# Kernel tuning notes

Hardware: AMD Instinct MI355X
Metric: run time of the kernel (lower is better)

## Reference

```python
import jax, jax.numpy as jnp
import numpy as np

B, S, H, K = 64, 512, 768, 21  # batch, seq_len, bert hidden, num_labels


def setup_inputs() -> dict:
    key = jax.random.key(0)
    ks = jax.random.split(key, 8)
    hidden = jax.random.normal(ks[0], (B, S, H), jnp.float32)  # post-BERT states
    W = jax.random.normal(ks[1], (H, K), jnp.float32) * 0.02    # classifier weight
    b = jnp.zeros((K,), jnp.float32)                            # classifier bias
    start_transitions = jax.random.uniform(ks[2], (K,), jnp.float32, -0.1, 0.1)
    transitions = jax.random.uniform(ks[3], (K, K), jnp.float32, -0.1, 0.1)
    end_transitions = jax.random.uniform(ks[4], (K,), jnp.float32, -0.1, 0.1)
    labels = jax.random.randint(ks[5], (B, S), 0, K)
    # torchcrf requires mask[:, 0] == 1; use variable-length prefix masks
    lengths = jax.random.randint(ks[6], (B,), S // 2, S + 1)
    attention_mask = jnp.arange(S)[None, :] < lengths[:, None]  # [B,S] bool
    return dict(hidden=hidden, W=W, b=b,
                start_transitions=start_transitions,
                transitions=transitions,
                end_transitions=end_transitions,
                labels=labels, attention_mask=attention_mask)


def _crf_nll(logits, labels, mask, start_t, trans, end_t):
    """torchcrf CRF forward (reduction='sum' log-likelihood), negated."""
    fmask = mask.astype(logits.dtype)  # [B,S]
    # ---- numerator: score of the gold path ----
    emit = jnp.take_along_axis(logits, labels[..., None], axis=2)[..., 0]  # [B,S]
    tr = trans[labels[:, :-1], labels[:, 1:]]                              # [B,S-1]
    num = start_t[labels[:, 0]] + emit[:, 0] \
        + jnp.sum((emit[:, 1:] + tr) * fmask[:, 1:], axis=1)
    lengths = mask.sum(axis=1)
    last_tags = jnp.take_along_axis(labels, (lengths - 1)[:, None], axis=1)[:, 0]
    num = num + end_t[last_tags]
    # ---- denominator: forward algorithm (logsumexp recurrence) ----
    alpha0 = start_t[None, :] + logits[:, 0]           # [B,K]
    ems = jnp.swapaxes(logits[:, 1:], 0, 1)            # [S-1,B,K]
    ms = jnp.swapaxes(mask[:, 1:], 0, 1)               # [S-1,B]

    def step(alpha, xs):
        em, m = xs
        nxt = jax.scipy.special.logsumexp(
            alpha[:, :, None] + trans[None, :, :] + em[:, None, :], axis=1)
        return jnp.where(m[:, None], nxt, alpha), None

    alpha, _ = jax.lax.scan(step, alpha0, (ems, ms))
    logZ = jax.scipy.special.logsumexp(alpha + end_t[None, :], axis=1)  # [B]
    return jnp.sum(logZ - num)  # negative log-likelihood (sum over batch)


def reference(hidden, W, b, start_transitions, transitions, end_transitions,
              labels, attention_mask):
    # dropout is identity in eval; the GRU in __init__ is unused in forward
    logits = hidden @ W + b  # [B,S,K]
    nll = _crf_nll(logits, labels, attention_mask,
                   start_transitions, transitions, end_transitions)
    # module returns (logits, -1 * log_likelihood) = (logits, nll)
    return (logits, nll)
```

## Files before the change

kernel.cpp:

```cpp
#include <hip/hip_runtime.h>

#define BSZ 64
#define SEQ 512
#define HID 768
#define NK  21
#define NSEG 64
#define SEGLEN 8

typedef short bf16x8 __attribute__((ext_vector_type(8)));
typedef float f32x4  __attribute__((ext_vector_type(4)));

__device__ __forceinline__ unsigned f2bf1(float x) {
    unsigned u = __float_as_uint(x);
    return (u + 0x7fffu + ((u >> 16) & 1u)) >> 16;
}
__device__ __forceinline__ unsigned f2bf_pk(float lo, float hi) {
    return f2bf1(lo) | (f2bf1(hi) << 16);
}

__global__ __launch_bounds__(256) void wconv_kernel(
    const float* __restrict__ W, unsigned short* __restrict__ WT)
{
    const int idx = blockIdx.x * 256 + threadIdx.x;
    const int n = idx / HID;
    const int k = idx - n * HID;
    unsigned short v = 0;
    if (n < NK) v = (unsigned short)f2bf1(W[(size_t)k * NK + n]);
    WT[idx] = v;
}

__global__ __launch_bounds__(256) void gemm_bias_kernel(
    const float* __restrict__ hidden, const unsigned short* __restrict__ WT,
    const float* __restrict__ bias, float* __restrict__ out)
{
    const int tid  = threadIdx.x;
    const int lane = tid & 63;
    const int wv   = tid >> 6;
    const int n    = lane & 15;
    const int quad = lane >> 4;

    const int arow = blockIdx.x * 64 + wv * 16 + n;
    const float* ap = hidden + (size_t)arow * HID + quad * 8;
    const bf16x8* bp0 = (const bf16x8*)(WT + (size_t)n * HID + quad * 8);
    const bf16x8* bp1 = (const bf16x8*)(WT + (size_t)(16 + n) * HID + quad * 8);

    f32x4 acc0 = {0.f, 0.f, 0.f, 0.f};
    f32x4 acc1 = {0.f, 0.f, 0.f, 0.f};

    float4 c0a = *(const float4*)(ap + 0);
    float4 c0b = *(const float4*)(ap + 4);

    #pragma unroll
    for (int c = 0; c < HID / 32; ++c) {
        float4 c1a, c1b;
        if (c + 1 < HID / 32) {
            c1a = *(const float4*)(ap + (c + 1) * 32);
            c1b = *(const float4*)(ap + (c + 1) * 32 + 4);
        }
        union { bf16x8 v; unsigned u[4]; } af;
        af.u[0] = f2bf_pk(c0a.x, c0a.y);
        af.u[1] = f2bf_pk(c0a.z, c0a.w);
        af.u[2] = f2bf_pk(c0b.x, c0b.y);
        af.u[3] = f2bf_pk(c0b.z, c0b.w);

        const bf16x8 b0 = bp0[c * 4];
        const bf16x8 b1 = bp1[c * 4];

        acc0 = __builtin_amdgcn_mfma_f32_16x16x32_bf16(af.v, b0, acc0, 0, 0, 0);
        acc1 = __builtin_amdgcn_mfma_f32_16x16x32_bf16(af.v, b1, acc1, 0, 0, 0);
        c0a = c1a; c0b = c1b;
    }

    const float b0v = bias[n];
    const float b1v = (n < NK - 16) ? bias[16 + n] : 0.f;
    const int rbase = blockIdx.x * 64 + wv * 16 + quad * 4;
    #pragma unroll
    for (int r = 0; r < 4; ++r) {
        float* op = out + (size_t)(rbase + r) * NK;
        op[n] = acc0[r] + b0v;
        if (n < NK - 16) op[16 + n] = acc1[r] + b1v;
    }
}

__global__ __launch_bounds__(64) void prepass_kernel(
    const float* __restrict__ logits, const float* __restrict__ trans,
    const int* __restrict__ mask,
    float* __restrict__ Nrow, float* __restrict__ Ncol,
    float* __restrict__ rlog)
{
    const int bs   = blockIdx.x;
    const int b    = bs >> 6;
    const int s    = bs & 63;
    const int lane = threadIdx.x;
    int g = lane / 21; if (g > 2) g = 2;
    int i = lane - g * 21; if (i > 20) i = 20;
    const int j0 = 7 * g;

    const int* msk = mask + b * SEQ;
    int cnt = 0;
    #pragma unroll
    for (int t = 0; t < SEQ / 64; ++t) cnt += (msk[lane + 64 * t] != 0);
    #pragma unroll
    for (int off = 32; off > 0; off >>= 1) cnt += __shfl_xor(cnt, off, 64);
    const int L = cnt;

    float E[21][7];
    #pragma unroll
    for (int k = 0; k < 21; ++k)
        #pragma unroll
        for (int jl = 0; jl < 7; ++jl)
            E[k][jl] = __expf(trans[k * NK + j0 + jl]);

    const float* lg = logits + (size_t)b * SEQ * NK;

    float P[7];
    float rl = 0.f;
    const int t0 = s * SEGLEN + 1;

    if (t0 < L) {
        const float C = lg[t0 * NK];
        #pragma unroll
        for (int jl = 0; jl < 7; ++jl)
            P[jl] = E[i][jl] * __expf(lg[t0 * NK + j0 + jl] - C);
    } else {
        #pragma unroll
        for (int jl = 0; jl < 7; ++jl) P[jl] = (i == j0 + jl) ? 1.f : 0.f;
    }

#define BPF(v, idx) __uint_as_float(__builtin_amdgcn_ds_bpermute((idx) * 4, __float_as_uint(v)))

    #pragma unroll
    for (int u = 1; u < SEGLEN; ++u) {
        const int t = t0 + u;
        if (t < L) {
            float row[21];
            #pragma unroll
            for (int k = 0; k < 21; ++k)
                row[k] = BPF(P[k % 7], (k / 7) * 21 + i);

            const float C = lg[t * NK];
            float X[7];
            #pragma unroll
            for (int jl = 0; jl < 7; ++jl)
                X[jl] = __expf(lg[t * NK + j0 + jl] - C);

            #pragma unroll
            for (int jl = 0; jl < 7; ++jl) {
                float s0 = row[0] * E[0][jl];
                float s1 = row[1] * E[1][jl];
                float s2 = row[2] * E[2][jl];
                #pragma unroll
                for (int k = 3; k < 21; k += 3) {
                    s0 = fmaf(row[k    ], E[k    ][jl], s0);
                    s1 = fmaf(row[k + 1], E[k + 1][jl], s1);
                    s2 = fmaf(row[k + 2], E[k + 2][jl], s2);
                }
                P[jl] = ((s0 + s1) + s2) * X[jl];
            }
            const float m = BPF(P[0], 0);
            const float r = __builtin_amdgcn_rcpf(m);
            #pragma unroll
            for (int jl = 0; jl < 7; ++jl) P[jl] *= r;
            rl += __logf(m);
        }
    }
#undef BPF

    if (lane < 63) {
        float* nr = Nrow + (size_t)bs * 441 + i * 21 + j0;
        #pragma unroll
        for (int jl = 0; jl < 7; ++jl) nr[jl] = P[jl];
        float* nc = Ncol + (size_t)bs * 441 + i;
        #pragma unroll
        for (int jl = 0; jl < 7; ++jl) nc[(j0 + jl) * 21] = P[jl];
    }
    if (lane == 0) rlog[bs] = rl;
}

__global__ __launch_bounds__(128) void scan_kernel(
    const float* __restrict__ logits,
    const float* __restrict__ start_t,
    const float* __restrict__ trans,
    const float* __restrict__ end_t,
    const int* __restrict__ labels,
    const int* __restrict__ mask,
    const float* __restrict__ Nrow, const float* __restrict__ Ncol,
    const float* __restrict__ rlog,
    float* __restrict__ per_batch)
{
    __shared__ float comb[26];

    const int b    = blockIdx.x;
    const int tid  = threadIdx.x;
    const int lane = tid & 63;
    const int wid  = tid >> 6;

    const float* lg = logits + (size_t)b * SEQ * NK;
    const int* lab = labels + b * SEQ;
    const int* msk = mask   + b * SEQ;

    int cnt = 0;
    #pragma unroll
    for (int t = 0; t < SEQ / 64; ++t) cnt += (msk[lane + 64 * t] != 0);
    #pragma unroll
    for (int off = 32; off > 0; off >>= 1) cnt += __shfl_xor(cnt, off, 64);
    const int L = cnt;

    {
        float numacc = 0.f;
        for (int t = tid; t < L; t += 128) {
            if (t == 0) numacc += start_t[lab[0]] + lg[lab[0]];
            else        numacc += lg[t * NK + lab[t]] + trans[lab[t - 1] * NK + lab[t]];
        }
        if (tid == 0) numacc += end_t[lab[L - 1]];
        #pragma unroll
        for (int off = 32; off > 0; off >>= 1) numacc += __shfl_xor(numacc, off, 64);
        if (lane == 0) comb[22 + wid] = numacc;
    }

    float rls = (lane < 32) ? rlog[b * NSEG + wid * 32 + lane] : 0.f;
    #pragma unroll
    for (int off = 32; off > 0; off >>= 1) rls += __shfl_xor(rls, off, 64);

    const int jj = (lane < NK) ? lane : NK - 1;

#define RL(v, k) __uint_as_float(__builtin_amdgcn_readlane(__float_as_uint(v), k))

    float a, csum = 0.f, Orenorm = 0.f;
    float ncur[21], nnx[21];

    if (wid == 0) {
        const int hi = (L < 256) ? L : 256;
        for (int t = lane; t < hi; t += 64) csum += lg[t * NK];
        a = __expf(start_t[jj]) * __expf(lg[jj] - lg[0]);

        const float* base = Ncol + (size_t)b * NSEG * 441 + jj * 21;
        #pragma unroll
        for (int k = 0; k < 21; ++k) ncur[k] = base[k];
        for (int s = 0; s < 32; ++s) {
            if (s < 31) {
                const float* p = base + (size_t)(s + 1) * 441;
                #pragma unroll
                for (int k = 0; k < 21; ++k) nnx[k] = p[k];
            }
            float s0 = RL(a, 0) * ncur[0];
            float s1 = RL(a, 1) * ncur[1];
            float s2 = RL(a, 2) * ncur[2];
            #pragma unroll
            for (int k = 3; k < 21; k += 3) {
                s0 = fmaf(RL(a, k    ), ncur[k    ], s0);
                s1 = fmaf(RL(a, k + 1), ncur[k + 1], s1);
                s2 = fmaf(RL(a, k + 2), ncur[k + 2], s2);
            }
            a = (s0 + s1) + s2;
            const float m = __uint_as_float(
                __builtin_amdgcn_readfirstlane(__float_as_uint(a)));
            a *= __builtin_amdgcn_rcpf(m);
            Orenorm += __logf(m);
            if (s < 31) {
                #pragma unroll
                for (int k = 0; k < 21; ++k) ncur[k] = nnx[k];
            }
        }
    } else {
        for (int t = 256 + lane; t < L; t += 64) csum += lg[t * NK];
        a = __expf(end_t[jj]);

        const float* base = Nrow + (size_t)b * NSEG * 441 + jj * 21;
        #pragma unroll
        for (int k = 0; k < 21; ++k) ncur[k] = base[(size_t)63 * 441 + k];
        for (int s = 63; s >= 32; --s) {
            if (s > 32) {
                const float* p = base + (size_t)(s - 1) * 441;
                #pragma unroll
                for (int k = 0; k < 21; ++k) nnx[k] = p[k];
            }
            float s0 = RL(a, 0) * ncur[0];
            float s1 = RL(a, 1) * ncur[1];
            float s2 = RL(a, 2) * ncur[2];
            #pragma unroll
            for (int k = 3; k < 21; k += 3) {
                s0 = fmaf(RL(a, k    ), ncur[k    ], s0);
                s1 = fmaf(RL(a, k + 1), ncur[k + 1], s1);
                s2 = fmaf(RL(a, k + 2), ncur[k + 2], s2);
            }
            a = (s0 + s1) + s2;
            const float m = __uint_as_float(
                __builtin_amdgcn_readfirstlane(__float_as_uint(a)));
            a *= __builtin_amdgcn_rcpf(m);
            Orenorm += __logf(m);
            if (s > 32) {
                #pragma unroll
                for (int k = 0; k < 21; ++k) ncur[k] = nnx[k];
            }
        }
    }
#undef RL

    #pragma unroll
    for (int off = 32; off > 0; off >>= 1) csum += __shfl_xor(csum, off, 64);

    if (wid == 1) {
        if (lane < NK) comb[lane] = a;
        if (lane == 0) comb[21] = csum + Orenorm + rls;
    }
    __syncthreads();

    if (wid == 0) {
        float val = (lane < NK) ? a * comb[lane] : 0.f;
        #pragma unroll
        for (int off = 32; off > 0; off >>= 1) val += __shfl_xor(val, off, 64);
        if (lane == 0) {
            const float OF  = csum + Orenorm + rls;
            const float num = comb[22] + comb[23];
            per_batch[b] = OF + comb[21] + __logf(val) - num;
        }
    }
}

__global__ __launch_bounds__(64) void reduce_kernel(
    const float* __restrict__ pb, float* __restrict__ out)
{
    float v = pb[threadIdx.x];
    #pragma unroll
    for (int off = 32; off > 0; off >>= 1) v += __shfl_xor(v, off, 64);
    if (threadIdx.x == 0) out[BSZ * SEQ * NK] = v;
}

extern "C" void kernel_launch(void* const* d_in, const int* in_sizes, int n_in,
                              void* d_out, int out_size, void* d_ws, size_t ws_size,
                              hipStream_t stream)
{
    const float* hidden  = (const float*)d_in[0];
    const float* W       = (const float*)d_in[1];
    const float* bias    = (const float*)d_in[2];
    const float* start_t = (const float*)d_in[3];
    const float* trans   = (const float*)d_in[4];
    const float* end_t   = (const float*)d_in[5];
    const int*   labels  = (const int*)d_in[6];
    const int*   mask    = (const int*)d_in[7];
    float* out = (float*)d_out;

    unsigned short* WT = (unsigned short*)d_ws;
    float* f    = (float*)((char*)d_ws + 65536);
    float* pb   = f;
    float* rlog = f + 64;
    float* Nrow = f + 8192;
    float* Ncol = Nrow + BSZ * NSEG * 441;

    wconv_kernel<<<(32 * HID) / 256, 256, 0, stream>>>(W, WT);
    gemm_bias_kernel<<<(BSZ * SEQ) / 64, 256, 0, stream>>>(hidden, WT, bias, out);
    prepass_kernel<<<BSZ * NSEG, 64, 0, stream>>>(out, trans, mask, Nrow, Ncol, rlog);
    scan_kernel<<<BSZ, 128, 0, stream>>>(out, start_t, trans, end_t, labels, mask,
                                         Nrow, Ncol, rlog, pb);
    reduce_kernel<<<1, 64, 0, stream>>>(pb, out);
}
```

Measured before the change: 245.2 us.

## Halve CRF segments, store segment matrices in bf16, precompute lengths once

```diff
diff --git a/kernel.cpp b/kernel.cpp
--- a/kernel.cpp
+++ b/kernel.cpp
@@ -4,8 +4,9 @@
 #define SEQ 512
 #define HID 768
 #define NK  21
-#define NSEG 64
-#define SEGLEN 8
+#define NSEG 32
+#define SEGLEN 16
+#define PSTR 448
 
 typedef short bf16x8 __attribute__((ext_vector_type(8)));
 typedef float f32x4  __attribute__((ext_vector_type(4)));
@@ -17,16 +18,31 @@
 __device__ __forceinline__ unsigned f2bf_pk(float lo, float hi) {
     return f2bf1(lo) | (f2bf1(hi) << 16);
 }
-
-__global__ __launch_bounds__(256) void wconv_kernel(
-    const float* __restrict__ W, unsigned short* __restrict__ WT)
-{
-    const int idx = blockIdx.x * 256 + threadIdx.x;
-    const int n = idx / HID;
-    const int k = idx - n * HID;
-    unsigned short v = 0;
-    if (n < NK) v = (unsigned short)f2bf1(W[(size_t)k * NK + n]);
-    WT[idx] = v;
+__device__ __forceinline__ float bf2f(unsigned short v) {
+    return __uint_as_float(((unsigned)v) << 16);
+}
+
+__global__ __launch_bounds__(256) void wconv_len_kernel(
+    const float* __restrict__ W, const int* __restrict__ mask,
+    unsigned short* __restrict__ WT, int* __restrict__ Lbuf)
+{
+    if (blockIdx.x < 96) {
+        const int idx = blockIdx.x * 256 + threadIdx.x;
+        const int n = idx / HID;
+        const int k = idx - n * HID;
+        unsigned short v = 0;
+        if (n < NK) v = (unsigned short)f2bf1(W[(size_t)k * NK + n]);
+        WT[idx] = v;
+    } else {
+        const int tid = threadIdx.x;
+        const int b = tid >> 2, q = tid & 3;
+        const int* msk = mask + b * SEQ + q * 128;
+        int cnt = 0;
+        for (int r = 0; r < 128; ++r) cnt += (msk[r] != 0);
+        cnt += __shfl_xor(cnt, 1, 64);
+        cnt += __shfl_xor(cnt, 2, 64);
+        if (q == 0) Lbuf[b] = cnt;
+    }
 }
 
 __global__ __launch_bounds__(256) void gemm_bias_kernel(
@@ -84,25 +100,19 @@
 
 __global__ __launch_bounds__(64) void prepass_kernel(
     const float* __restrict__ logits, const float* __restrict__ trans,
-    const int* __restrict__ mask,
-    float* __restrict__ Nrow, float* __restrict__ Ncol,
+    const int* __restrict__ Lbuf,
+    unsigned short* __restrict__ Nrowb, unsigned short* __restrict__ Ncolb,
     float* __restrict__ rlog)
 {
     const int bs   = blockIdx.x;
-    const int b    = bs >> 6;
-    const int s    = bs & 63;
+    const int b    = bs >> 5;
+    const int s    = bs & 31;
     const int lane = threadIdx.x;
     int g = lane / 21; if (g > 2) g = 2;
     int i = lane - g * 21; if (i > 20) i = 20;
     const int j0 = 7 * g;
 
-    const int* msk = mask + b * SEQ;
-    int cnt = 0;
-    #pragma unroll
-    for (int t = 0; t < SEQ / 64; ++t) cnt += (msk[lane + 64 * t] != 0);
-    #pragma unroll
-    for (int off = 32; off > 0; off >>= 1) cnt += __shfl_xor(cnt, off, 64);
-    const int L = cnt;
+    const int L = Lbuf[b];
 
     float E[21][7];
     #pragma unroll
@@ -167,12 +177,13 @@
 #undef BPF
 
     if (lane < 63) {
-        float* nr = Nrow + (size_t)bs * 441 + i * 21 + j0;
-        #pragma unroll
-        for (int jl = 0; jl < 7; ++jl) nr[jl] = P[jl];
-        float* nc = Ncol + (size_t)bs * 441 + i;
-        #pragma unroll
-        for (int jl = 0; jl < 7; ++jl) nc[(j0 + jl) * 21] = P[jl];
+        unsigned short* nr = Nrowb + (size_t)bs * PSTR + i * 21 + j0;
+        #pragma unroll
+        for (int jl = 0; jl < 7; ++jl) nr[jl] = (unsigned short)f2bf1(P[jl]);
+        unsigned short* nc = Ncolb + (size_t)bs * PSTR + i;
+        #pragma unroll
+        for (int jl = 0; jl < 7; ++jl)
+            nc[(j0 + jl) * 21] = (unsigned short)f2bf1(P[jl]);
     }
     if (lane == 0) rlog[bs] = rl;
 }
@@ -183,8 +194,9 @@
     const float* __restrict__ trans,
     const float* __restrict__ end_t,
     const int* __restrict__ labels,
-    const int* __restrict__ mask,
-    const float* __restrict__ Nrow, const float* __restrict__ Ncol,
+    const int* __restrict__ Lbuf,
+    const unsigned short* __restrict__ Nrowb,
+    const unsigned short* __restrict__ Ncolb,
     const float* __restrict__ rlog,
     float* __restrict__ per_batch)
 {
@@ -197,14 +209,7 @@
 
     const float* lg = logits + (size_t)b * SEQ * NK;
     const int* lab = labels + b * SEQ;
-    const int* msk = mask   + b * SEQ;
-
-    int cnt = 0;
-    #pragma unroll
-    for (int t = 0; t < SEQ / 64; ++t) cnt += (msk[lane + 64 * t] != 0);
-    #pragma unroll
-    for (int off = 32; off > 0; off >>= 1) cnt += __shfl_xor(cnt, off, 64);
-    const int L = cnt;
+    const int L = Lbuf[b];
 
     {
         float numacc = 0.f;
@@ -218,7 +223,7 @@
         if (lane == 0) comb[22 + wid] = numacc;
     }
 
-    float rls = (lane < 32) ? rlog[b * NSEG + wid * 32 + lane] : 0.f;
+    float rls = (lane < 16) ? rlog[b * NSEG + wid * 16 + lane] : 0.f;
     #pragma unroll
     for (int off = 32; off > 0; off >>= 1) rls += __shfl_xor(rls, off, 64);
 
@@ -230,18 +235,17 @@
     float ncur[21], nnx[21];
 
     if (wid == 0) {
-        const int hi = (L < 256) ? L : 256;
-        for (int t = lane; t < hi; t += 64) csum += lg[t * NK];
+        for (int t = lane; t < 256; t += 64) csum += lg[t * NK];
         a = __expf(start_t[jj]) * __expf(lg[jj] - lg[0]);
 
-        const float* base = Ncol + (size_t)b * NSEG * 441 + jj * 21;
-        #pragma unroll
-        for (int k = 0; k < 21; ++k) ncur[k] = base[k];
-        for (int s = 0; s < 32; ++s) {
-            if (s < 31) {
-                const float* p = base + (size_t)(s + 1) * 441;
-                #pragma unroll
-                for (int k = 0; k < 21; ++k) nnx[k] = p[k];
+        const unsigned short* base = Ncolb + (size_t)b * NSEG * PSTR + jj * 21;
+        #pragma unroll
+        for (int k = 0; k < 21; ++k) ncur[k] = bf2f(base[k]);
+        for (int s = 0; s < 16; ++s) {
+            if (s < 15) {
+                const unsigned short* p = base + (size_t)(s + 1) * PSTR;
+                #pragma unroll
+                for (int k = 0; k < 21; ++k) nnx[k] = bf2f(p[k]);
             }
             float s0 = RL(a, 0) * ncur[0];
             float s1 = RL(a, 1) * ncur[1];
@@ -257,7 +261,7 @@
                 __builtin_amdgcn_readfirstlane(__float_as_uint(a)));
             a *= __builtin_amdgcn_rcpf(m);
             Orenorm += __logf(m);
-            if (s < 31) {
+            if (s < 15) {
                 #pragma unroll
                 for (int k = 0; k < 21; ++k) ncur[k] = nnx[k];
             }
@@ -266,14 +270,14 @@
         for (int t = 256 + lane; t < L; t += 64) csum += lg[t * NK];
         a = __expf(end_t[jj]);
 
-        const float* base = Nrow + (size_t)b * NSEG * 441 + jj * 21;
-        #pragma unroll
-        for (int k = 0; k < 21; ++k) ncur[k] = base[(size_t)63 * 441 + k];
-        for (int s = 63; s >= 32; --s) {
-            if (s > 32) {
-                const float* p = base + (size_t)(s - 1) * 441;
-                #pragma unroll
-                for (int k = 0; k < 21; ++k) nnx[k] = p[k];
+        const unsigned short* base = Nrowb + (size_t)b * NSEG * PSTR + jj * 21;
+        #pragma unroll
+        for (int k = 0; k < 21; ++k) ncur[k] = bf2f(base[(size_t)31 * PSTR + k]);
+        for (int s = 31; s >= 16; --s) {
+            if (s > 16) {
+                const unsigned short* p = base + (size_t)(s - 1) * PSTR;
+                #pragma unroll
+                for (int k = 0; k < 21; ++k) nnx[k] = bf2f(p[k]);
             }
             float s0 = RL(a, 0) * ncur[0];
             float s1 = RL(a, 1) * ncur[1];
@@ -289,7 +293,7 @@
                 __builtin_amdgcn_readfirstlane(__float_as_uint(a)));
             a *= __builtin_amdgcn_rcpf(m);
             Orenorm += __logf(m);
-            if (s > 32) {
+            if (s > 16) {
                 #pragma unroll
                 for (int k = 0; k < 21; ++k) ncur[k] = nnx[k];
             }
@@ -341,17 +345,18 @@
     const int*   mask    = (const int*)d_in[7];
     float* out = (float*)d_out;
 
-    unsigned short* WT = (unsigned short*)d_ws;
-    float* f    = (float*)((char*)d_ws + 65536);
-    float* pb   = f;
-    float* rlog = f + 64;
-    float* Nrow = f + 8192;
-    float* Ncol = Nrow + BSZ * NSEG * 441;
-
-    wconv_kernel<<<(32 * HID) / 256, 256, 0, stream>>>(W, WT);
+    char* ws = (char*)d_ws;
+    unsigned short* WT    = (unsigned short*)ws;
+    float*          pb    = (float*)(ws + 65536);
+    int*            Lbuf  = (int*)(ws + 66560);
+    float*          rlog  = (float*)(ws + 69632);
+    unsigned short* Nrowb = (unsigned short*)(ws + 131072);
+    unsigned short* Ncolb = (unsigned short*)(ws + 131072 + 2097152);
+
+    wconv_len_kernel<<<97, 256, 0, stream>>>(W, mask, WT, Lbuf);
     gemm_bias_kernel<<<(BSZ * SEQ) / 64, 256, 0, stream>>>(hidden, WT, bias, out);
-    prepass_kernel<<<BSZ * NSEG, 64, 0, stream>>>(out, trans, mask, Nrow, Ncol, rlog);
-    scan_kernel<<<BSZ, 128, 0, stream>>>(out, start_t, trans, end_t, labels, mask,
-                                         Nrow, Ncol, rlog, pb);
+    prepass_kernel<<<BSZ * NSEG, 64, 0, stream>>>(out, trans, Lbuf, Nrowb, Ncolb, rlog);
+    scan_kernel<<<BSZ, 128, 0, stream>>>(out, start_t, trans, end_t, labels, Lbuf,
+                                         Nrowb, Ncolb, rlog, pb);
     reduce_kernel<<<1, 64, 0, stream>>>(pb, out);
 }
```

After: 228.6 us. 6.7% less time.
